# Optimization experiments

Measured on AMD Instinct MI355X. Metric: run time of the kernel, lower is better.

Reference implementation:

```python
import jax, jax.numpy as jnp
import numpy as np

B, N = 16, 1024
NT = 3            # atom types
NPT = 6           # pair types = NT*(NT+1)//2


def setup_inputs() -> dict:
    key = jax.random.key(0)
    ks = jax.random.split(key, 8)
    types = jax.random.randint(ks[0], (B, N), 0, NT, dtype=jnp.int32)
    n_atoms = jax.random.randint(ks[1], (B,), N // 2, N + 1, dtype=jnp.int32)
    # interatomic distances in a physically plausible range [1.5, 5.5)
    distances = 1.5 + 4.0 * jax.random.uniform(ks[2], (B, N, N), dtype=jnp.float32)
    # pair type index from (ti, tj) using combinations_with_replacement ordering
    ti = types[:, :, None]
    tj = types[:, None, :]
    lo = jnp.minimum(ti, tj)
    hi = jnp.maximum(ti, tj)
    pair_types = (lo * (2 * NT - lo + 1) // 2 + (hi - lo)).astype(jnp.int32)
    # per-pair-type potential params [a, b, r0] and density params [xi, q, r0]
    phi_params = jnp.stack([
        0.5 + jax.random.uniform(ks[3], (NPT,)),          # a
        1.0 + jax.random.uniform(ks[4], (NPT,)),          # b
        2.0 + jax.random.uniform(ks[5], (NPT,)),          # r0
    ], axis=-1).astype(jnp.float32)
    rho_params = jnp.stack([
        0.5 + jax.random.uniform(ks[6], (NPT,)),          # xi
        1.0 + jax.random.uniform(ks[7], (NPT,)),          # q
        2.0 + jax.random.uniform(jax.random.fold_in(key, 9), (NPT,)),  # r0
    ], axis=-1).astype(jnp.float32)
    emb_params = jnp.stack([
        0.5 + jax.random.uniform(jax.random.fold_in(key, 10), (NT,)),  # A (sqrt embedding)
        0.1 * jax.random.normal(jax.random.fold_in(key, 11), (NT,)),   # offset
    ], axis=-1).astype(jnp.float32)
    return {"types": types, "n_atoms": n_atoms, "distances": distances,
            "pair_types": pair_types, "phi_params": phi_params,
            "rho_params": rho_params, "emb_params": emb_params}


def reference(types, n_atoms, distances, pair_types, phi_params, rho_params, emb_params):
    # masks emulating raggedness: valid atoms and valid (i != j) pairs
    idx = jnp.arange(N)
    atom_mask = idx[None, :] < n_atoms[:, None]                      # [B, N]
    pair_mask = (atom_mask[:, :, None] & atom_mask[:, None, :]
                 & ~jnp.eye(N, dtype=bool)[None])                    # [B, N, N]

    # per-pair-type routed potential and density (branchless 'where' method)
    pp = phi_params[pair_types]                                      # [B, N, N, 3]
    phi = pp[..., 0] * jnp.exp(-pp[..., 1] * (distances - pp[..., 2]))
    rp = rho_params[pair_types]
    rho = rp[..., 0] * jnp.exp(-rp[..., 1] * (distances - rp[..., 2]))
    phi = jnp.where(pair_mask, phi, 0.0)
    rho = jnp.where(pair_mask, rho, 0.0)

    # scatter/reduce over neighbors -> per-atom quantities
    sum_rho = jnp.sum(rho * rho, axis=-1)                            # [B, N]
    sum_phi = jnp.sum(phi, axis=-1)                                  # [B, N]
    sum_rho = jnp.maximum(sum_rho, 1e-30)

    # per-atom-type embedding F(|x|) + offset
    A = emb_params[types, 0]
    off = emb_params[types, 1]
    emb = -A * jnp.sqrt(jnp.abs(sum_rho)) + off

    atomic_energies = jnp.where(atom_mask, sum_phi + emb, 0.0)       # [B, N]
    energy = jnp.sum(atomic_energies, axis=-1, keepdims=True)        # [B, 1]
    energy_per_atom = energy / n_atoms[:, None].astype(energy.dtype)
    return energy_per_atom
```

## Files before the change

kernel.cpp:

```cpp
#include <hip/hip_runtime.h>

#define NN 1024
#define BB 16
#define NTY 3

__global__ __launch_bounds__(256) void eam_rows(
    const int* __restrict__ types, const int* __restrict__ n_atoms,
    const float* __restrict__ distances,
    const float* __restrict__ phi_params, const float* __restrict__ rho_params,
    const float* __restrict__ emb_params, float* __restrict__ row_e)
{
    __shared__ int4  s_types4[NN / 4];
    __shared__ float4 s_tbl[NTY * NTY];

    const int tid = threadIdx.x;
    const int b = blockIdx.y;
    const int rowBase = blockIdx.x * 8;

    s_types4[tid] = ((const int4*)(types + b * NN))[tid];

    if (tid < NTY * NTY) {
        const int ti = tid / NTY, tj = tid % NTY;
        const int lo = min(ti, tj), hi = max(ti, tj);
        const int pt = lo * (2 * NTY - lo + 1) / 2 + (hi - lo);
        const float p0 = phi_params[pt * 3 + 0];
        const float p1 = phi_params[pt * 3 + 1];
        const float p2 = phi_params[pt * 3 + 2];
        const float r0 = rho_params[pt * 3 + 0];
        const float r1 = rho_params[pt * 3 + 1];
        const float r2 = rho_params[pt * 3 + 2];
        const float LOG2E = 1.44269504088896f;
        s_tbl[tid] = make_float4(p0 * __expf(p1 * p2), -p1 * LOG2E,
                                 r0 * __expf(r1 * r2), -r1 * LOG2E);
    }
    __syncthreads();

    const int lane = tid & 63;
    const int wave = tid >> 6;
    const int na = n_atoms[b];
    const int* s_types = (const int*)s_types4;

#pragma unroll
    for (int rr = 0; rr < 2; ++rr) {
        const int i = rowBase + wave * 2 + rr;
        if (i < na) {
            const int ti = s_types[i];
            const float4* drow =
                (const float4*)(distances + ((size_t)(b * NN + i)) * NN);
            float sph = 0.f, srh = 0.f;
#pragma unroll
            for (int pass = 0; pass < 4; ++pass) {
                const int c4 = pass * 64 + lane;
                const float4 d4 = drow[c4];
                const int4 tj4 = s_types4[c4];
                const int jb = c4 * 4;

#define EAM_EL(E, DD, TT)                                                     \
                {                                                             \
                    const float4 prm = s_tbl[ti * NTY + (TT)];                \
                    float phi = prm.x * __builtin_amdgcn_exp2f(prm.y * (DD)); \
                    float rho = prm.z * __builtin_amdgcn_exp2f(prm.w * (DD)); \
                    const int j = jb + (E);                                   \
                    if (j >= na || j == i) { phi = 0.f; rho = 0.f; }          \
                    sph += phi;                                               \
                    srh += rho * rho;                                         \
                }
                EAM_EL(0, d4.x, tj4.x)
                EAM_EL(1, d4.y, tj4.y)
                EAM_EL(2, d4.z, tj4.z)
                EAM_EL(3, d4.w, tj4.w)
#undef EAM_EL
            }
#pragma unroll
            for (int o = 32; o > 0; o >>= 1) {
                sph += __shfl_xor(sph, o, 64);
                srh += __shfl_xor(srh, o, 64);
            }
            if (lane == 0) {
                const float A   = emb_params[ti * 2 + 0];
                const float off = emb_params[ti * 2 + 1];
                row_e[b * NN + i] =
                    sph + (-A * sqrtf(fmaxf(srh, 1e-30f)) + off);
            }
        } else {
            if (lane == 0) row_e[b * NN + i] = 0.f;
        }
    }
}

__global__ __launch_bounds__(256) void eam_reduce(
    const float* __restrict__ row_e, const int* __restrict__ n_atoms,
    float* __restrict__ out)
{
    const int b = blockIdx.x;
    const int tid = threadIdx.x;
    const float4 v = ((const float4*)(row_e + b * NN))[tid];
    float s = v.x + v.y + v.z + v.w;
#pragma unroll
    for (int o = 32; o > 0; o >>= 1) s += __shfl_xor(s, o, 64);

    __shared__ float wsum[4];
    const int lane = tid & 63, wave = tid >> 6;
    if (lane == 0) wsum[wave] = s;
    __syncthreads();
    if (tid == 0) {
        const float t = wsum[0] + wsum[1] + wsum[2] + wsum[3];
        out[b] = t / (float)n_atoms[b];
    }
}

extern "C" void kernel_launch(void* const* d_in, const int* in_sizes, int n_in,
                              void* d_out, int out_size, void* d_ws, size_t ws_size,
                              hipStream_t stream) {
    const int*   types      = (const int*)d_in[0];
    const int*   n_atoms    = (const int*)d_in[1];
    const float* distances  = (const float*)d_in[2];
    const float* phi_params = (const float*)d_in[4];
    const float* rho_params = (const float*)d_in[5];
    const float* emb_params = (const float*)d_in[6];

    float* row_e = (float*)d_ws;

    eam_rows<<<dim3(NN / 8, BB), 256, 0, stream>>>(
        types, n_atoms, distances, phi_params, rho_params, emb_params, row_e);
    eam_reduce<<<BB, 256, 0, stream>>>(row_e, n_atoms, (float*)d_out);
}
```

Baseline: 19.79 us.

## Fuse row and batch reductions with atomic last-block finalize, skip padded columns

Merges the per-row energy kernel and the per-batch reduce kernel into one launch. Each block sums its eight row energies in shared memory, atomically adds the total to a per-batch accumulator, and the last block to arrive (found with an atomic counter) writes energy divided by n_atoms. The column loop now stops after ceil(n_atoms/256) passes and prefetches the next distance vector one pass ahead. The rho table is folded to a squared amplitude with a doubled exponent, so the per-element square is dropped. The change adds a memset launch and float atomics, which make the summation order nondeterministic.

```diff
diff --git a/kernel.cpp b/kernel.cpp
--- a/kernel.cpp
+++ b/kernel.cpp
@@ -3,15 +3,19 @@
 #define NN 1024
 #define BB 16
 #define NTY 3
+#define BLOCKS_PER_BATCH (NN / 8)
 
-__global__ __launch_bounds__(256) void eam_rows(
+__global__ __launch_bounds__(256) void eam_fused(
     const int* __restrict__ types, const int* __restrict__ n_atoms,
     const float* __restrict__ distances,
     const float* __restrict__ phi_params, const float* __restrict__ rho_params,
-    const float* __restrict__ emb_params, float* __restrict__ row_e)
+    const float* __restrict__ emb_params,
+    float* __restrict__ ws_acc, int* __restrict__ ws_cnt,
+    float* __restrict__ out)
 {
-    __shared__ int4  s_types4[NN / 4];
+    __shared__ int4   s_types4[NN / 4];
     __shared__ float4 s_tbl[NTY * NTY];
+    __shared__ float  s_rowe[8];
 
     const int tid = threadIdx.x;
     const int b = blockIdx.y;
@@ -30,45 +34,50 @@
         const float r1 = rho_params[pt * 3 + 1];
         const float r2 = rho_params[pt * 3 + 2];
         const float LOG2E = 1.44269504088896f;
+        const float ra = r0 * __expf(r1 * r2);
         s_tbl[tid] = make_float4(p0 * __expf(p1 * p2), -p1 * LOG2E,
-                                 r0 * __expf(r1 * r2), -r1 * LOG2E);
+                                 ra * ra, -2.0f * r1 * LOG2E);
     }
     __syncthreads();
 
     const int lane = tid & 63;
     const int wave = tid >> 6;
     const int na = n_atoms[b];
+    const int npass = (na + 255) >> 8;
     const int* s_types = (const int*)s_types4;
 
 #pragma unroll
     for (int rr = 0; rr < 2; ++rr) {
         const int i = rowBase + wave * 2 + rr;
+        float rowE = 0.f;
         if (i < na) {
             const int ti = s_types[i];
             const float4* drow =
                 (const float4*)(distances + ((size_t)(b * NN + i)) * NN);
             float sph = 0.f, srh = 0.f;
-#pragma unroll
-            for (int pass = 0; pass < 4; ++pass) {
+
+            float4 d4 = drow[lane];
+            for (int pass = 0; pass < npass; ++pass) {
                 const int c4 = pass * 64 + lane;
-                const float4 d4 = drow[c4];
+                const float4 cur = d4;
+                if (pass + 1 < npass) d4 = drow[c4 + 64];
                 const int4 tj4 = s_types4[c4];
                 const int jb = c4 * 4;
 
 #define EAM_EL(E, DD, TT)                                                     \
                 {                                                             \
                     const float4 prm = s_tbl[ti * NTY + (TT)];                \
-                    float phi = prm.x * __builtin_amdgcn_exp2f(prm.y * (DD)); \
-                    float rho = prm.z * __builtin_amdgcn_exp2f(prm.w * (DD)); \
+                    float phi  = prm.x * __builtin_amdgcn_exp2f(prm.y * (DD));\
+                    float rho2 = prm.z * __builtin_amdgcn_exp2f(prm.w * (DD));\
                     const int j = jb + (E);                                   \
-                    if (j >= na || j == i) { phi = 0.f; rho = 0.f; }          \
+                    if (j >= na || j == i) { phi = 0.f; rho2 = 0.f; }         \
                     sph += phi;                                               \
-                    srh += rho * rho;                                         \
+                    srh += rho2;                                              \
                 }
-                EAM_EL(0, d4.x, tj4.x)
-                EAM_EL(1, d4.y, tj4.y)
-                EAM_EL(2, d4.z, tj4.z)
-                EAM_EL(3, d4.w, tj4.w)
+                EAM_EL(0, cur.x, tj4.x)
+                EAM_EL(1, cur.y, tj4.y)
+                EAM_EL(2, cur.z, tj4.z)
+                EAM_EL(3, cur.w, tj4.w)
 #undef EAM_EL
             }
 #pragma unroll
@@ -76,36 +85,25 @@
                 sph += __shfl_xor(sph, o, 64);
                 srh += __shfl_xor(srh, o, 64);
             }
-            if (lane == 0) {
-                const float A   = emb_params[ti * 2 + 0];
-                const float off = emb_params[ti * 2 + 1];
-                row_e[b * NN + i] =
-                    sph + (-A * sqrtf(fmaxf(srh, 1e-30f)) + off);
-            }
-        } else {
-            if (lane == 0) row_e[b * NN + i] = 0.f;
+            const float A   = emb_params[ti * 2 + 0];
+            const float off = emb_params[ti * 2 + 1];
+            rowE = sph + (-A * sqrtf(fmaxf(srh, 1e-30f)) + off);
         }
+        if (lane == 0) s_rowe[wave * 2 + rr] = rowE;
     }
-}
+    __syncthreads();
 
-__global__ __launch_bounds__(256) void eam_reduce(
-    const float* __restrict__ row_e, const int* __restrict__ n_atoms,
-    float* __restrict__ out)
-{
-    const int b = blockIdx.x;
-    const int tid = threadIdx.x;
-    const float4 v = ((const float4*)(row_e + b * NN))[tid];
-    float s = v.x + v.y + v.z + v.w;
+    if (tid == 0) {
+        float s = 0.f;
 #pragma unroll
-    for (int o = 32; o > 0; o >>= 1) s += __shfl_xor(s, o, 64);
-
-    __shared__ float wsum[4];
-    const int lane = tid & 63, wave = tid >> 6;
-    if (lane == 0) wsum[wave] = s;
-    __syncthreads();
-    if (tid == 0) {
-        const float t = wsum[0] + wsum[1] + wsum[2] + wsum[3];
-        out[b] = t / (float)n_atoms[b];
+        for (int k = 0; k < 8; ++k) s += s_rowe[k];
+        atomicAdd(&ws_acc[b], s);
+        __threadfence();
+        const int old = atomicAdd(&ws_cnt[b], 1);
+        if (old == BLOCKS_PER_BATCH - 1) {
+            const float tot = atomicAdd(&ws_acc[b], 0.0f);
+            out[b] = tot / (float)na;
+        }
     }
 }
 
@@ -119,9 +117,12 @@
     const float* rho_params = (const float*)d_in[5];
     const float* emb_params = (const float*)d_in[6];
 
-    float* row_e = (float*)d_ws;
+    float* ws_acc = (float*)d_ws;
+    int*   ws_cnt = (int*)((char*)d_ws + BB * sizeof(float));
 
-    eam_rows<<<dim3(NN / 8, BB), 256, 0, stream>>>(
-        types, n_atoms, distances, phi_params, rho_params, emb_params, row_e);
-    eam_reduce<<<BB, 256, 0, stream>>>(row_e, n_atoms, (float*)d_out);
+    hipMemsetAsync(d_ws, 0, BB * (sizeof(float) + sizeof(int)), stream);
+
+    eam_fused<<<dim3(BLOCKS_PER_BATCH, BB), 256, 0, stream>>>(
+        types, n_atoms, distances, phi_params, rho_params, emb_params,
+        ws_acc, ws_cnt, (float*)d_out);
 }
```

Result: slower. 71.18 us (+259.7%).
